# Kernel optimization log

Hardware: AMD Instinct MI355X
Metric: run time of the kernel (lower is better)

The kernel has to match this reference:

```python
import math
import jax, jax.numpy as jnp
import numpy as np

B, T, C = 2, 2048, 1024
HEADS = 16
HD = C // HEADS  # 64


def setup_inputs() -> dict:
    key = jax.random.key(0)
    ks = jax.random.split(key, 5)
    s = 0.02
    return {
        "x": jax.random.normal(ks[0], (B, T, C), jnp.float32),
        "Wq": jax.random.normal(ks[1], (C, C), jnp.float32) * s,
        "bq": jnp.zeros((C,), jnp.float32),
        "Wk": jax.random.normal(ks[2], (C, HD), jnp.float32) * s,
        "bk": jnp.zeros((HD,), jnp.float32),
        "Wv": jax.random.normal(ks[3], (C, HD), jnp.float32) * s,
        "bv": jnp.zeros((HD,), jnp.float32),
        "Wo": jax.random.normal(ks[4], (C, C), jnp.float32) * s,
        "bo": jnp.zeros((C,), jnp.float32),
    }


def _rope_tables(seq_len, dim):
    pos = jnp.arange(seq_len, dtype=jnp.float32)
    freqs = 1.0 / (10000.0 ** (jnp.arange(0, dim, 2, dtype=jnp.float32) / dim))
    ang = pos[:, None] * freqs[None, :]          # (T, dim//2)
    # broadcast over (B, T, H, dim//2)
    return jnp.sin(ang)[None, :, None, :], jnp.cos(ang)[None, :, None, :]


def _apply_rope(t, sin, cos, dim):
    t1, t2 = t[..., : dim // 2], t[..., dim // 2 :]
    # matches torch source: emb[..., :d/2]=sin, emb[..., d/2:]=cos
    return jnp.concatenate([t1 * cos + t2 * sin, t1 * sin - t2 * cos], axis=-1)


def reference(x, Wq, bq, Wk, bk, Wv, bv, Wo, bo):
    Bx, Tx, Cx = x.shape
    q = (x @ Wq + bq).reshape(Bx, Tx, HEADS, HD)   # (B,T,H,hd)
    k = (x @ Wk + bk)[:, :, None, :]               # (B,T,1,hd) single KV head (MQA)
    v = (x @ Wv + bv)[:, :, None, :]
    sin, cos = _rope_tables(Tx, HD)
    q = _apply_rope(q, sin, cos, HD)
    k = _apply_rope(k, sin, cos, HD)
    att = jnp.einsum('bthd,bThd->bhtT', q, k) / math.sqrt(HD)
    causal = jnp.triu(jnp.ones((Tx, Tx), bool), 1)
    att = jnp.where(causal, -jnp.inf, att)
    att = jax.nn.softmax(att, axis=-1)
    out = jnp.einsum('bhtT,bThd->bthd', att, v).reshape(Bx, Tx, Cx)
    return out @ Wo + bo
```

## Files before the change

### kernel.cpp

```cpp
#include <hip/hip_runtime.h>
#include <math.h>

#define BSZ   2
#define TSEQ  2048
#define CDIM  1024
#define NHEAD 16
#define HDIM  64
#define BT    (BSZ*TSEQ)
#define NQKV  1152

typedef __attribute__((ext_vector_type(8))) short short8;
typedef __attribute__((ext_vector_type(4))) float f32x4;
typedef unsigned short u16;
typedef unsigned int   u32;

__device__ __forceinline__ u16 f2b(float f) {
    union { float f; u32 u; } c; c.f = f;
    u32 u = c.u;
    u += 0x7fffu + ((u >> 16) & 1u);
    return (u16)(u >> 16);
}
__device__ __forceinline__ u32 pack2(float lo, float hi) {
    return (u32)f2b(lo) | ((u32)f2b(hi) << 16);
}

__device__ __forceinline__ void async_copy16(const void* g, void* l) {
    __builtin_amdgcn_global_load_lds(
        (__attribute__((address_space(1))) const void*)g,
        (__attribute__((address_space(3))) void*)l,
        16, 0, 0);
}

__global__ __launch_bounds__(256) void cast_bf16_kernel(
    const float* __restrict__ src, u16* __restrict__ dst, int n4)
{
    int i = blockIdx.x * 256 + threadIdx.x;
    if (i >= n4) return;
    float4 f = ((const float4*)src)[i];
    u16* d = dst + (size_t)i * 4;
    d[0] = f2b(f.x); d[1] = f2b(f.y); d[2] = f2b(f.z); d[3] = f2b(f.w);
}

__global__ __launch_bounds__(256) void transpose_cast_kernel(
    const float* __restrict__ W, u16* __restrict__ Wt,
    int K, int Nw, int nofs)
{
    __shared__ float T[64][65];
    const int tid = threadIdx.x;
    const int k0 = blockIdx.y * 64, n0 = blockIdx.x * 64;
    #pragma unroll
    for (int i = 0; i < 16; ++i) {
        int idx = i * 256 + tid, r = idx >> 6, c = idx & 63;
        T[r][c] = W[(size_t)(k0 + r) * Nw + n0 + c];
    }
    __syncthreads();
    #pragma unroll
    for (int i = 0; i < 16; ++i) {
        int idx = i * 256 + tid, rn = idx >> 6, ck = idx & 63;
        Wt[(size_t)(nofs + n0 + rn) * K + k0 + ck] = f2b(T[ck][rn]);
    }
}

__global__ __launch_bounds__(256) void concat_bias3_kernel(
    const float* __restrict__ bq, const float* __restrict__ bk,
    const float* __restrict__ bv, float* __restrict__ bqkv)
{
    int i = blockIdx.x * 256 + threadIdx.x;
    if (i >= NQKV) return;
    bqkv[i] = (i < 1024) ? bq[i] : (i < 1088 ? bk[i - 1024] : bv[i - 1088]);
}

__global__ __launch_bounds__(256) void gemm_mfma_kernel(
    const u16* __restrict__ A, const u16* __restrict__ Bt,
    const float* __restrict__ bias, float* __restrict__ Y,
    int M, int N, int K)
{
    __shared__ __align__(16) u16 AsC[64 * 32];
    __shared__ __align__(16) u16 BsC[128 * 32];
    const int tid  = threadIdx.x;
    const int wave = tid >> 6, lane = tid & 63;
    const int ln16 = lane & 15, quad = lane >> 4;
    const int wm = wave >> 1, wn = wave & 1;
    const int m0 = blockIdx.y * 64, n0 = blockIdx.x * 128;

    const int c_row = ((tid >> 6) << 4) + (tid & 15);
    const int c_k   = ((tid >> 4) & 3) * 8;
    const u16* ag  = &A [(size_t)(m0 + c_row)       * K + c_k];
    const u16* bg0 = &Bt[(size_t)(n0 + c_row)       * K + c_k];
    const u16* bg1 = &Bt[(size_t)(n0 + 64 + c_row)  * K + c_k];
    u16* a_l  = &AsC[(size_t)wave * 64 * 8];
    u16* b_l0 = &BsC[(size_t)wave * 64 * 8];
    u16* b_l1 = &BsC[(size_t)(wave + 4) * 64 * 8];

    f32x4 acc[2][4];
    #pragma unroll
    for (int i = 0; i < 2; ++i)
        #pragma unroll
        for (int j = 0; j < 4; ++j) acc[i][j] = (f32x4){0.f, 0.f, 0.f, 0.f};

    for (int k0 = 0; k0 < K; k0 += 32) {
        async_copy16(ag,  a_l);
        async_copy16(bg0, b_l0);
        async_copy16(bg1, b_l1);
        ag += 32; bg0 += 32; bg1 += 32;
        __syncthreads();

        short8 af[2], bf[4];
        #pragma unroll
        for (int mt = 0; mt < 2; ++mt)
            af[mt] = *(const short8*)&AsC[(((wm * 2 + mt) * 64) + quad * 16 + ln16) * 8];
        #pragma unroll
        for (int nt = 0; nt < 4; ++nt)
            bf[nt] = *(const short8*)&BsC[(((wn * 4 + nt) * 64) + quad * 16 + ln16) * 8];
        #pragma unroll
        for (int mt = 0; mt < 2; ++mt)
            #pragma unroll
            for (int nt = 0; nt < 4; ++nt)
                acc[mt][nt] = __builtin_amdgcn_mfma_f32_16x16x32_bf16(
                    af[mt], bf[nt], acc[mt][nt], 0, 0, 0);
        __syncthreads();
    }

    #pragma unroll
    for (int mt = 0; mt < 2; ++mt)
        #pragma unroll
        for (int nt = 0; nt < 4; ++nt) {
            int n = n0 + wn * 64 + nt * 16 + ln16;
            float bb = bias[n];
            #pragma unroll
            for (int r = 0; r < 4; ++r) {
                int m = m0 + wm * 32 + mt * 16 + quad * 4 + r;
                Y[(size_t)m * N + n] = acc[mt][nt][r] + bb;
            }
        }
}

__global__ __launch_bounds__(256) void rope_qk_kernel(
    const float* __restrict__ qkvf, u16* __restrict__ qb, u16* __restrict__ kb)
{
    int idx = blockIdx.x * 256 + threadIdx.x;
    const int total = BT * 17 * 16;
    if (idx >= total) return;
    int p4  = idx & 15;
    int rest = idx >> 4;
    int hh  = rest % 17;
    int bt  = rest / 17;
    int j   = p4 * 2;
    int tpos = bt & (TSEQ - 1);
    float f0 = exp2f(-0.41524101186092029f * (float)j);
    float f1 = exp2f(-0.41524101186092029f * (float)(j + 1));
    float a0s, a0c, a1s, a1c;
    __sincosf((float)tpos * f0, &a0s, &a0c);
    __sincosf((float)tpos * f1, &a1s, &a1c);
    const float* base = qkvf + (size_t)bt * NQKV + hh * 64;
    float t10 = base[j],      t11 = base[j + 1];
    float t20 = base[j + 32], t21 = base[j + 33];
    float lo0 = fmaf(t10, a0c, t20 * a0s), lo1 = fmaf(t11, a1c, t21 * a1s);
    float hi0 = fmaf(t10, a0s, -t20 * a0c), hi1 = fmaf(t11, a1s, -t21 * a1c);
    if (hh < 16) {
        u16* o = qb + (size_t)bt * CDIM + hh * 64 + j;
        *(u32*)o        = pack2(lo0 * 0.125f, lo1 * 0.125f);
        *(u32*)(o + 32) = pack2(hi0 * 0.125f, hi1 * 0.125f);
    } else {
        u16* o = kb + (size_t)bt * HDIM + j;
        *(u32*)o        = pack2(lo0, lo1);
        *(u32*)(o + 32) = pack2(hi0, hi1);
    }
}

__global__ __launch_bounds__(256) void transpose_v_kernel(
    const float* __restrict__ qkvf, u16* __restrict__ vT)
{
    __shared__ float T[64][65];
    const int tid = threadIdx.x;
    const int b  = blockIdx.y;
    const int t0 = blockIdx.x * 64;
    #pragma unroll
    for (int i = 0; i < 16; ++i) {
        int idx = i * 256 + tid, r = idx >> 6, c = idx & 63;
        T[r][c] = qkvf[(size_t)(b * TSEQ + t0 + r) * NQKV + 1088 + c];
    }
    __syncthreads();
    #pragma unroll
    for (int i = 0; i < 8; ++i) {
        int idx = i * 256 + tid;
        int d = idx >> 5, tp = idx & 31;
        u32 u = pack2(T[tp * 2][d], T[tp * 2 + 1][d]);
        *(u32*)&vT[(size_t)(b * HDIM + d) * TSEQ + t0 + tp * 2] = u;
    }
}

__global__ __launch_bounds__(256) void flash_mfma_kernel(
    const u16* __restrict__ qb, const u16* __restrict__ kb,
    const u16* __restrict__ vT, u16* __restrict__ o)
{
    const int id = blockIdx.x;
    const int p  = id & 15;
    const int h  = (id >> 4) & 15;
    const int b  = id >> 8;
    __shared__ __align__(16) u16 Qs[512 * 8];
    __shared__ __align__(16) u16 Ks[512 * 8];
    __shared__ __align__(16) u16 Vs[512 * 8];
    __shared__ __align__(16) u16 Ps[4 * 16 * 72];

    const int tid  = threadIdx.x;
    const int wave = tid >> 6, lane = tid & 63;
    const int ln16 = lane & 15, quad = lane >> 4;

    const int c0 = tid;
    int row_c[2], off_c[2];
    #pragma unroll
    for (int hf = 0; hf < 2; ++hf) {
        int c = c0 + hf * 256;
        row_c[hf] = ((c >> 7) << 4) | (c & 15);
        off_c[hf] = ((c >> 6) & 1) * 32 + ((c >> 4) & 3) * 8;
    }

    u16* Pw = &Ps[wave * 16 * 72];

    for (int s = 0; s < 2; ++s) {
        const int qt = s ? (31 - p) : p;

        #pragma unroll
        for (int hf = 0; hf < 2; ++hf)
            async_copy16(
                qb + (size_t)(b * TSEQ + qt * 64 + row_c[hf]) * CDIM + h * HDIM + off_c[hf],
                Qs + (c0 + hf * 256) * 8);

        float lsum[4];
        f32x4 oacc[4];
        #pragma unroll
        for (int r = 0; r < 4; ++r) lsum[r] = 0.f;
        #pragma unroll
        for (int t = 0; t < 4; ++t) oacc[t] = (f32x4){0.f, 0.f, 0.f, 0.f};

        for (int kt = 0; kt <= qt; ++kt) {
            const size_t kt0 = (size_t)(b * TSEQ + kt * 64);
            #pragma unroll
            for (int hf = 0; hf < 2; ++hf) {
                int cc = c0 + hf * 256;
                async_copy16(kb + (kt0 + row_c[hf]) * HDIM + off_c[hf], Ks + cc * 8);
                async_copy16(vT + (size_t)(b * HDIM + row_c[hf]) * TSEQ + kt * 64 + off_c[hf],
                             Vs + cc * 8);
            }
            __syncthreads();

            f32x4 sv[4];
            #pragma unroll
            for (int t = 0; t < 4; ++t) sv[t] = (f32x4){0.f, 0.f, 0.f, 0.f};
            #pragma unroll
            for (int kk2 = 0; kk2 < 2; ++kk2) {
                short8 af = *(const short8*)&Qs[(wave * 128 + kk2 * 64 + quad * 16 + ln16) * 8];
                #pragma unroll
                for (int t = 0; t < 4; ++t) {
                    short8 bf = *(const short8*)&Ks[(t * 128 + kk2 * 64 + quad * 16 + ln16) * 8];
                    sv[t] = __builtin_amdgcn_mfma_f32_16x16x32_bf16(af, bf, sv[t], 0, 0, 0);
                }
            }

            if (kt == qt) {
                #pragma unroll
                for (int t = 0; t < 4; ++t) {
                    int key = t * 16 + ln16;
                    #pragma unroll
                    for (int r = 0; r < 4; ++r) {
                        float e = (key > wave * 16 + quad * 4 + r)
                                    ? 0.f : __expf(sv[t][r]);
                        lsum[r] += e;
                        Pw[(quad * 4 + r) * 72 + t * 16 + ln16] = f2b(e);
                    }
                }
            } else {
                #pragma unroll
                for (int t = 0; t < 4; ++t)
                    #pragma unroll
                    for (int r = 0; r < 4; ++r) {
                        float e = __expf(sv[t][r]);
                        lsum[r] += e;
                        Pw[(quad * 4 + r) * 72 + t * 16 + ln16] = f2b(e);
                    }
            }

            #pragma unroll
            for (int kk2 = 0; kk2 < 2; ++kk2) {
                short8 pf = *(const short8*)&Pw[ln16 * 72 + kk2 * 32 + quad * 8];
                #pragma unroll
                for (int t = 0; t < 4; ++t) {
                    short8 vf = *(const short8*)&Vs[(t * 128 + kk2 * 64 + quad * 16 + ln16) * 8];
                    oacc[t] = __builtin_amdgcn_mfma_f32_16x16x32_bf16(pf, vf, oacc[t], 0, 0, 0);
                }
            }
            __syncthreads();
        }

        float inv[4];
        #pragma unroll
        for (int r = 0; r < 4; ++r) {
            float l = lsum[r];
            #pragma unroll
            for (int off = 1; off < 16; off <<= 1)
                l += __shfl_xor(l, off, 64);
            inv[r] = 1.0f / l;
        }
        #pragma unroll
        for (int t = 0; t < 4; ++t) {
            #pragma unroll
            for (int r = 0; r < 4; ++r) {
                int row = qt * 64 + wave * 16 + quad * 4 + r;
                int d   = t * 16 + ln16;
                o[(size_t)(b * TSEQ + row) * CDIM + h * HDIM + d] = f2b(oacc[t][r] * inv[r]);
            }
        }
    }
}

extern "C" void kernel_launch(void* const* d_in, const int* in_sizes, int n_in,
                              void* d_out, int out_size, void* d_ws, size_t ws_size,
                              hipStream_t stream)
{
    const float* x  = (const float*)d_in[0];
    const float* Wq = (const float*)d_in[1];
    const float* bq = (const float*)d_in[2];
    const float* Wk = (const float*)d_in[3];
    const float* bk = (const float*)d_in[4];
    const float* Wv = (const float*)d_in[5];
    const float* bv = (const float*)d_in[6];
    const float* Wo = (const float*)d_in[7];
    const float* bo = (const float*)d_in[8];
    float* out = (float*)d_out;

    const size_t MB = 1u << 20;
    char* w = (char*)d_ws;
    u16*   xb   = (u16*)(w);
    u16*   qb   = (u16*)(w);
    float* qkvf = (float*)(w + 8 * MB);
    u16*   aob  = (u16*)(w + 8 * MB);
    u16*   Wqkvt= (u16*)(w + 26 * MB);
    u16*   Wot  = (u16*)(w + 29 * MB);
    u16*   kb   = (u16*)(w + 31 * MB);
    u16*   vT   = (u16*)(w + 31 * MB + 512 * 1024);
    float* bqkv = (float*)(w + 32 * MB);

    dim3 blk(256);

    cast_bf16_kernel<<<dim3(BT * CDIM / 4 / 256), blk, 0, stream>>>(x, xb, BT * CDIM / 4);
    transpose_cast_kernel<<<dim3(16, 16), blk, 0, stream>>>(Wq, Wqkvt, CDIM, CDIM, 0);
    transpose_cast_kernel<<<dim3(1, 16),  blk, 0, stream>>>(Wk, Wqkvt, CDIM, HDIM, 1024);
    transpose_cast_kernel<<<dim3(1, 16),  blk, 0, stream>>>(Wv, Wqkvt, CDIM, HDIM, 1088);
    transpose_cast_kernel<<<dim3(16, 16), blk, 0, stream>>>(Wo, Wot, CDIM, CDIM, 0);
    concat_bias3_kernel<<<dim3(5), blk, 0, stream>>>(bq, bk, bv, bqkv);

    gemm_mfma_kernel<<<dim3(NQKV / 128, BT / 64), blk, 0, stream>>>(
        xb, Wqkvt, bqkv, qkvf, BT, NQKV, CDIM);

    rope_qk_kernel<<<dim3(BT * 17 * 16 / 256), blk, 0, stream>>>(qkvf, qb, kb);
    transpose_v_kernel<<<dim3(TSEQ / 64, BSZ), blk, 0, stream>>>(qkvf, vT);

    flash_mfma_kernel<<<dim3(16 * NHEAD * BSZ), blk, 0, stream>>>(qb, kb, vT, aob);

    gemm_mfma_kernel<<<dim3(CDIM / 128, BT / 64), blk, 0, stream>>>(
        aob, Wot, bo, out, BT, CDIM, CDIM);
}
```

Baseline: 223.1 us.

## Fuse RoPE and V transpose into QKV GEMM epilogue; merge prep kernels

Moves the RoPE rotation, the Q scaling, the bf16 cast and the V transpose into the epilogue of the QKV GEMM, so the fp32 qkv intermediate is no longer written to and read back from global memory. It also merges the four weight transpose/cast launches and the bias concat into one prep kernel. Together these drop about five kernel launches and roughly 18 MB of intermediate traffic. In exchange, the epilogue's scattered 2-byte stores to qb/kb are less coalesced and each element computes its own sincos.

```diff
diff --git a/kernel.cpp b/kernel.cpp
--- a/kernel.cpp
+++ b/kernel.cpp
@@ -41,13 +41,12 @@
     d[0] = f2b(f.x); d[1] = f2b(f.y); d[2] = f2b(f.z); d[3] = f2b(f.w);
 }
 
-__global__ __launch_bounds__(256) void transpose_cast_kernel(
+__device__ __forceinline__ void transpose_tile(
     const float* __restrict__ W, u16* __restrict__ Wt,
-    int K, int Nw, int nofs)
-{
-    __shared__ float T[64][65];
+    int K, int Nw, int nofs, int bx, int by, float (*T)[65])
+{
     const int tid = threadIdx.x;
-    const int k0 = blockIdx.y * 64, n0 = blockIdx.x * 64;
+    const int k0 = by * 64, n0 = bx * 64;
     #pragma unroll
     for (int i = 0; i < 16; ++i) {
         int idx = i * 256 + tid, r = idx >> 6, c = idx & 63;
@@ -61,19 +60,34 @@
     }
 }
 
-__global__ __launch_bounds__(256) void concat_bias3_kernel(
+__global__ __launch_bounds__(256) void prep_kernel(
+    const float* __restrict__ Wq, const float* __restrict__ Wk,
+    const float* __restrict__ Wv, const float* __restrict__ Wo,
     const float* __restrict__ bq, const float* __restrict__ bk,
-    const float* __restrict__ bv, float* __restrict__ bqkv)
-{
-    int i = blockIdx.x * 256 + threadIdx.x;
-    if (i >= NQKV) return;
-    bqkv[i] = (i < 1024) ? bq[i] : (i < 1088 ? bk[i - 1024] : bv[i - 1088]);
-}
-
-__global__ __launch_bounds__(256) void gemm_mfma_kernel(
+    const float* __restrict__ bv,
+    u16* __restrict__ Wqkvt, u16* __restrict__ Wot, float* __restrict__ bqkv)
+{
+    __shared__ float T[64][65];
+    const int bid = blockIdx.x;
+    if (bid < 256) {
+        transpose_tile(Wq, Wqkvt, 1024, 1024, 0, bid & 15, bid >> 4, T);
+    } else if (bid < 272) {
+        transpose_tile(Wk, Wqkvt, 1024, 64, 1024, 0, bid - 256, T);
+    } else if (bid < 288) {
+        transpose_tile(Wv, Wqkvt, 1024, 64, 1088, 0, bid - 272, T);
+    } else if (bid < 544) {
+        int b2 = bid - 288;
+        transpose_tile(Wo, Wot, 1024, 1024, 0, b2 & 15, b2 >> 4, T);
+    } else {
+        for (int i = threadIdx.x; i < NQKV; i += 256)
+            bqkv[i] = (i < 1024) ? bq[i] : (i < 1088 ? bk[i - 1024] : bv[i - 1088]);
+    }
+}
+
+__global__ __launch_bounds__(256) void gemm_qkv_kernel(
     const u16* __restrict__ A, const u16* __restrict__ Bt,
-    const float* __restrict__ bias, float* __restrict__ Y,
-    int M, int N, int K)
+    const float* __restrict__ bias,
+    u16* __restrict__ qb, u16* __restrict__ kb, u16* __restrict__ vT)
 {
     __shared__ __align__(16) u16 AsC[64 * 32];
     __shared__ __align__(16) u16 BsC[128 * 32];
@@ -82,6 +96,7 @@
     const int ln16 = lane & 15, quad = lane >> 4;
     const int wm = wave >> 1, wn = wave & 1;
     const int m0 = blockIdx.y * 64, n0 = blockIdx.x * 128;
+    const int K = CDIM;
 
     const int c_row = ((tid >> 6) << 4) + (tid & 15);
     const int c_k   = ((tid >> 4) & 3) * 8;
@@ -125,6 +140,121 @@
     for (int mt = 0; mt < 2; ++mt)
         #pragma unroll
         for (int nt = 0; nt < 4; ++nt) {
+            float bb = bias[n0 + wn * 64 + nt * 16 + ln16];
+            #pragma unroll
+            for (int r = 0; r < 4; ++r) acc[mt][nt][r] += bb;
+        }
+
+    const int col0 = n0 + wn * 64;
+    if (col0 < 1024) {
+        const int hh = col0 >> 6;
+        #pragma unroll
+        for (int nt = 0; nt < 2; ++nt) {
+            int j = nt * 16 + ln16;
+            float fr = exp2f(-0.41524101186092029f * (float)j);
+            #pragma unroll
+            for (int mt = 0; mt < 2; ++mt)
+                #pragma unroll
+                for (int r = 0; r < 4; ++r) {
+                    int m = m0 + wm * 32 + mt * 16 + quad * 4 + r;
+                    float sn, cs;
+                    __sincosf((float)(m & (TSEQ - 1)) * fr, &sn, &cs);
+                    float t1 = acc[mt][nt][r], t2 = acc[mt][nt + 2][r];
+                    u16* o = qb + (size_t)m * CDIM + hh * 64 + j;
+                    o[0]  = f2b(fmaf(t1, cs,  t2 * sn) * 0.125f);
+                    o[32] = f2b(fmaf(t1, sn, -t2 * cs) * 0.125f);
+                }
+        }
+    } else if (wn == 0) {
+        #pragma unroll
+        for (int nt = 0; nt < 2; ++nt) {
+            int j = nt * 16 + ln16;
+            float fr = exp2f(-0.41524101186092029f * (float)j);
+            #pragma unroll
+            for (int mt = 0; mt < 2; ++mt)
+                #pragma unroll
+                for (int r = 0; r < 4; ++r) {
+                    int m = m0 + wm * 32 + mt * 16 + quad * 4 + r;
+                    float sn, cs;
+                    __sincosf((float)(m & (TSEQ - 1)) * fr, &sn, &cs);
+                    float t1 = acc[mt][nt][r], t2 = acc[mt][nt + 2][r];
+                    u16* o = kb + (size_t)m * HDIM + j;
+                    o[0]  = f2b(fmaf(t1, cs,  t2 * sn));
+                    o[32] = f2b(fmaf(t1, sn, -t2 * cs));
+                }
+        }
+    } else {
+        #pragma unroll
+        for (int nt = 0; nt < 4; ++nt) {
+            int d = nt * 16 + ln16;
+            #pragma unroll
+            for (int mt = 0; mt < 2; ++mt) {
+                int mr = m0 + wm * 32 + mt * 16 + quad * 4;
+                int b  = mr >> 11, tq = mr & (TSEQ - 1);
+                uint2 val;
+                val.x = pack2(acc[mt][nt][0], acc[mt][nt][1]);
+                val.y = pack2(acc[mt][nt][2], acc[mt][nt][3]);
+                *(uint2*)&vT[(size_t)(b * HDIM + d) * TSEQ + tq] = val;
+            }
+        }
+    }
+}
+
+__global__ __launch_bounds__(256) void gemm_mfma_kernel(
+    const u16* __restrict__ A, const u16* __restrict__ Bt,
+    const float* __restrict__ bias, float* __restrict__ Y,
+    int M, int N, int K)
+{
+    __shared__ __align__(16) u16 AsC[64 * 32];
+    __shared__ __align__(16) u16 BsC[128 * 32];
+    const int tid  = threadIdx.x;
+    const int wave = tid >> 6, lane = tid & 63;
+    const int ln16 = lane & 15, quad = lane >> 4;
+    const int wm = wave >> 1, wn = wave & 1;
+    const int m0 = blockIdx.y * 64, n0 = blockIdx.x * 128;
+
+    const int c_row = ((tid >> 6) << 4) + (tid & 15);
+    const int c_k   = ((tid >> 4) & 3) * 8;
+    const u16* ag  = &A [(size_t)(m0 + c_row)       * K + c_k];
+    const u16* bg0 = &Bt[(size_t)(n0 + c_row)       * K + c_k];
+    const u16* bg1 = &Bt[(size_t)(n0 + 64 + c_row)  * K + c_k];
+    u16* a_l  = &AsC[(size_t)wave * 64 * 8];
+    u16* b_l0 = &BsC[(size_t)wave * 64 * 8];
+    u16* b_l1 = &BsC[(size_t)(wave + 4) * 64 * 8];
+
+    f32x4 acc[2][4];
+    #pragma unroll
+    for (int i = 0; i < 2; ++i)
+        #pragma unroll
+        for (int j = 0; j < 4; ++j) acc[i][j] = (f32x4){0.f, 0.f, 0.f, 0.f};
+
+    for (int k0 = 0; k0 < K; k0 += 32) {
+        async_copy16(ag,  a_l);
+        async_copy16(bg0, b_l0);
+        async_copy16(bg1, b_l1);
+        ag += 32; bg0 += 32; bg1 += 32;
+        __syncthreads();
+
+        short8 af[2], bf[4];
+        #pragma unroll
+        for (int mt = 0; mt < 2; ++mt)
+            af[mt] = *(const short8*)&AsC[(((wm * 2 + mt) * 64) + quad * 16 + ln16) * 8];
+        #pragma unroll
+        for (int nt = 0; nt < 4; ++nt)
+            bf[nt] = *(const short8*)&BsC[(((wn * 4 + nt) * 64) + quad * 16 + ln16) * 8];
+        #pragma unroll
+        for (int mt = 0; mt < 2; ++mt)
+            #pragma unroll
+            for (int nt = 0; nt < 4; ++nt)
+                acc[mt][nt] = __builtin_amdgcn_mfma_f32_16x16x32_bf16(
+                    af[mt], bf[nt], acc[mt][nt], 0, 0, 0);
+        __syncthreads();
+    }
+
+    #pragma unroll
+    for (int mt = 0; mt < 2; ++mt)
+        #pragma unroll
+        for (int nt = 0; nt < 4; ++nt) {
             int n = n0 + wn * 64 + nt * 16 + ln16;
             float bb = bias[n];
             #pragma unroll
@@ -133,61 +263,6 @@
                 Y[(size_t)m * N + n] = acc[mt][nt][r] + bb;
             }
         }
-}
-
-__global__ __launch_bounds__(256) void rope_qk_kernel(
-    const float* __restrict__ qkvf, u16* __restrict__ qb, u16* __restrict__ kb)
-{
-    int idx = blockIdx.x * 256 + threadIdx.x;
-    const int total = BT * 17 * 16;
-    if (idx >= total) return;
-    int p4  = idx & 15;
-    int rest = idx >> 4;
-    int hh  = rest % 17;
-    int bt  = rest / 17;
-    int j   = p4 * 2;
-    int tpos = bt & (TSEQ - 1);
-    float f0 = exp2f(-0.41524101186092029f * (float)j);
-    float f1 = exp2f(-0.41524101186092029f * (float)(j + 1));
-    float a0s, a0c, a1s, a1c;
-    __sincosf((float)tpos * f0, &a0s, &a0c);
-    __sincosf((float)tpos * f1, &a1s, &a1c);
-    const float* base = qkvf + (size_t)bt * NQKV + hh * 64;
-    float t10 = base[j],      t11 = base[j + 1];
-    float t20 = base[j + 32], t21 = base[j + 33];
-    float lo0 = fmaf(t10, a0c, t20 * a0s), lo1 = fmaf(t11, a1c, t21 * a1s);
-    float hi0 = fmaf(t10, a0s, -t20 * a0c), hi1 = fmaf(t11, a1s, -t21 * a1c);
-    if (hh < 16) {
-        u16* o = qb + (size_t)bt * CDIM + hh * 64 + j;
-        *(u32*)o        = pack2(lo0 * 0.125f, lo1 * 0.125f);
-        *(u32*)(o + 32) = pack2(hi0 * 0.125f, hi1 * 0.125f);
-    } else {
-        u16* o = kb + (size_t)bt * HDIM + j;
-        *(u32*)o        = pack2(lo0, lo1);
-        *(u32*)(o + 32) = pack2(hi0, hi1);
-    }
-}
-
-__global__ __launch_bounds__(256) void transpose_v_kernel(
-    const float* __restrict__ qkvf, u16* __restrict__ vT)
-{
-    __shared__ float T[64][65];
-    const int tid = threadIdx.x;
-    const int b  = blockIdx.y;
-    const int t0 = blockIdx.x * 64;
-    #pragma unroll
-    for (int i = 0; i < 16; ++i) {
-        int idx = i * 256 + tid, r = idx >> 6, c = idx & 63;
-        T[r][c] = qkvf[(size_t)(b * TSEQ + t0 + r) * NQKV + 1088 + c];
-    }
-    __syncthreads();
-    #pragma unroll
-    for (int i = 0; i < 8; ++i) {
-        int idx = i * 256 + tid;
-        int d = idx >> 5, tp = idx & 31;
-        u32 u = pack2(T[tp * 2][d], T[tp * 2 + 1][d]);
-        *(u32*)&vT[(size_t)(b * HDIM + d) * TSEQ + t0 + tp * 2] = u;
-    }
 }
 
 __global__ __launch_bounds__(256) void flash_mfma_kernel(
@@ -332,32 +407,22 @@
     const size_t MB = 1u << 20;
     char* w = (char*)d_ws;
     u16*   xb   = (u16*)(w);
-    u16*   qb   = (u16*)(w);
-    float* qkvf = (float*)(w + 8 * MB);
-    u16*   aob  = (u16*)(w + 8 * MB);
-    u16*   Wqkvt= (u16*)(w + 26 * MB);
-    u16*   Wot  = (u16*)(w + 29 * MB);
-    u16*   kb   = (u16*)(w + 31 * MB);
-    u16*   vT   = (u16*)(w + 31 * MB + 512 * 1024);
-    float* bqkv = (float*)(w + 32 * MB);
+    u16*   aob  = (u16*)(w);
+    u16*   qb   = (u16*)(w + 8 * MB);
+    u16*   kb   = (u16*)(w + 16 * MB);
+    u16*   vT   = (u16*)(w + 16 * MB + 512 * 1024);
+    u16*   Wqkvt= (u16*)(w + 17 * MB);
+    u16*   Wot  = (u16*)(w + 20 * MB);
+    float* bqkv = (float*)(w + 22 * MB);
 
     dim3 blk(256);
 
     cast_bf16_kernel<<<dim3(BT * CDIM / 4 / 256), blk, 0, stream>>>(x, xb, BT * CDIM / 4);
-    transpose_cast_kernel<<<dim3(16, 16), blk, 0, stream>>>(Wq, Wqkvt, CDIM, CDIM, 0);
-    transpose_cast_kernel<<<dim3(1, 16),  blk, 0, stream>>>(Wk, Wqkvt, CDIM, HDIM, 1024);
-    transpose_cast_kernel<<<dim3(1, 16),  blk, 0, stream>>>(Wv, Wqkvt, CDIM, HDIM, 1088);
-    transpose_cast_kernel<<<dim3(16, 16), blk, 0, stream>>>(Wo, Wot, CDIM, CDIM, 0);
-    concat_bias3_kernel<<<dim3(5), blk, 0, stream>>>(bq, bk, bv, bqkv);
-
-    gemm_mfma_kernel<<<dim3(NQKV / 128, BT / 64), blk, 0, stream>>>(
-        xb, Wqkvt, bqkv, qkvf, BT, NQKV, CDIM);
-
-    rope_qk_kernel<<<dim3(BT * 17 * 16 / 256), blk, 0, stream>>>(qkvf, qb, kb);
-    transpose_v_kernel<<<dim3(TSEQ / 64, BSZ), blk, 0, stream>>>(qkvf, vT);
-
+    prep_kernel<<<dim3(545), blk, 0, stream>>>(Wq, Wk, Wv, Wo, bq, bk, bv,
+                                               Wqkvt, Wot, bqkv);
+    gemm_qkv_kernel<<<dim3(NQKV / 128, BT / 64), blk, 0, stream>>>(
+        xb, Wqkvt, bqkv, qb, kb, vT);
     flash_mfma_kernel<<<dim3(16 * NHEAD * BSZ), blk, 0, stream>>>(qb, kb, vT, aob);
-
     gemm_mfma_kernel<<<dim3(CDIM / 128, BT / 64), blk, 0, stream>>>(
         aob, Wot, bo, out, BT, CDIM, CDIM);
 }
```

New measurement: 205.0 us. 8.1% less time.
